# Optimization experiments

Measured on AMD Instinct MI355X. Metric: run time of the kernel, lower is better.

The kernel has to match this reference:

```python
import jax, jax.numpy as jnp
import numpy as np

DECAY = 0.999
EPS = 1e-05
COMMIT = 0.25


def _layer_norm(x, g, b, eps=1e-5):
    mu = x.mean(-1, keepdims=True)
    var = ((x - mu) ** 2).mean(-1, keepdims=True)
    return (x - mu) * jax.lax.rsqrt(var + eps) * g + b


def setup_inputs() -> dict:
    key = jax.random.key(0)
    ks = jax.random.split(key, 8)
    B, T, D, M, H = 8, 4096, 512, 1024, 512
    init_bound = 1.0 / 512
    embedding = jax.random.uniform(ks[0], (M, D), jnp.float32, -init_bound, init_bound)
    return {
        "dense_x": jax.random.normal(ks[1], (B, T, D), jnp.float32),
        "dense_padding_mask": jax.random.randint(ks[2], (B, T), 0, 2).astype(bool),
        "labels": jax.random.randint(ks[3], (B, T), 0, M),
        "embedding": embedding,
        "ema_count": jnp.zeros((M,), jnp.float32),
        "ema_weight": embedding,
        "ln1_g": jnp.ones((D,), jnp.float32),
        "ln1_b": jnp.zeros((D,), jnp.float32),
        "W1": jax.random.normal(ks[4], (D, H), jnp.float32) * (1.0 / np.sqrt(D)),
        "ln2_g": jnp.ones((H,), jnp.float32),
        "ln2_b": jnp.zeros((H,), jnp.float32),
        "W2": jax.random.normal(ks[5], (H, M), jnp.float32) * (1.0 / np.sqrt(H)),
    }


def reference(dense_x, dense_padding_mask, labels, embedding, ema_count, ema_weight,
              ln1_g, ln1_b, W1, ln2_g, ln2_b, W2):
    B, T, D = dense_x.shape
    M = embedding.shape[0]
    N = B * T

    # ---- VQ codebook (EMA) ----
    x_flat = jax.lax.stop_gradient(dense_x).reshape(N, D)
    distances = (jnp.sum(embedding ** 2, axis=1)[None, :]
                 + jnp.sum(x_flat ** 2, axis=1, keepdims=True)
                 - 2.0 * (x_flat @ embedding.T))
    indices = jnp.argmin(distances, axis=-1)  # [N]
    quantized = embedding[indices].reshape(B, T, D)

    # EMA codebook update (training path); encodings.sum(0) and encodings.T @ x
    # expressed as scatter-adds instead of materializing [N, M] one-hot.
    counts = jnp.zeros((M,), dense_x.dtype).at[indices].add(1.0)
    new_count = DECAY * ema_count + (1.0 - DECAY) * counts
    n = jnp.sum(new_count)
    new_count = (new_count + EPS) / (n + M * EPS) * n
    dw = jnp.zeros((M, D), dense_x.dtype).at[indices].add(x_flat)
    new_weight = DECAY * ema_weight + (1.0 - DECAY) * dw
    new_embedding = new_weight / new_count[:, None]

    e_latent_loss = (dense_x - jax.lax.stop_gradient(quantized)) ** 2  # [B,T,D]
    vq_loss = COMMIT * e_latent_loss
    quantized_st = dense_x + jax.lax.stop_gradient(quantized - dense_x)

    avg_probs = counts / N
    perplexity = jnp.exp(-jnp.sum(avg_probs * jnp.log(avg_probs + 1e-10)))

    # ---- decoder: LN -> ReLU -> Linear -> LN -> ReLU -> Linear ----
    h = jax.nn.relu(_layer_norm(dense_x, ln1_g, ln1_b)) @ W1      # [B,T,H]
    logits = jax.nn.relu(_layer_norm(h, ln2_g, ln2_b)) @ W2       # [B,T,M]

    # ---- cross-entropy with ignore_index=-1 (padding) ----
    lab = jnp.where(dense_padding_mask, -1, labels)
    valid = lab >= 0
    safe = jnp.where(valid, lab, 0)
    logp = jax.nn.log_softmax(logits, axis=-1)
    ce = -jnp.take_along_axis(logp, safe[..., None], axis=-1)[..., 0]
    recon_loss = jnp.where(valid, ce, 0.0)

    loss = recon_loss + vq_loss.sum(-1)  # [B,T]
    return quantized_st, loss, perplexity, new_embedding, new_count, new_weight
```

## Files before the change

kernel.cpp:

```cpp
#include <hip/hip_runtime.h>


#define N_TOK 32768

typedef __attribute__((ext_vector_type(8))) short short8;
typedef _Float16 half8 __attribute__((ext_vector_type(8)));
typedef __attribute__((ext_vector_type(4))) float f32x4;

__device__ __forceinline__ f32x4 mfma16(short8 a, short8 b, f32x4 c) {
    return __builtin_amdgcn_mfma_f32_16x16x32_bf16(a, b, c, 0, 0, 0);
}
__device__ __forceinline__ f32x4 mfma16h(half8 a, half8 b, f32x4 c) {
    return __builtin_amdgcn_mfma_f32_16x16x32_f16(a, b, c, 0, 0, 0);
}

__device__ __forceinline__ void gl_lds16(const void* g, void* l) {
    __builtin_amdgcn_global_load_lds(
        (const __attribute__((address_space(1))) void*)g,
        (__attribute__((address_space(3))) void*)l, 16, 0, 0);
}

__device__ __forceinline__ unsigned short f2bf(float x) {
    unsigned u = __float_as_uint(x);
    u += 0x7fffu + ((u >> 16) & 1u);
    return (unsigned short)(u >> 16);
}
__device__ __forceinline__ float bf2f(unsigned short h) {
    return __uint_as_float(((unsigned)h) << 16);
}
__device__ __forceinline__ unsigned short f2h(float x) {
    union { _Float16 h; unsigned short u; } c;
    c.h = (_Float16)x;
    return c.u;
}
__device__ __forceinline__ float h2f(unsigned short u) {
    union { _Float16 h; unsigned short u; } c;
    c.u = u;
    return (float)c.h;
}

__device__ __forceinline__ float waveSum(float v) {
#pragma unroll
    for (int off = 32; off > 0; off >>= 1) v += __shfl_down(v, off, 64);
    return v;
}
__device__ __forceinline__ float xorSum(float v) {
#pragma unroll
    for (int off = 1; off < 64; off <<= 1) v += __shfl_xor(v, off);
    return v;
}

__device__ __forceinline__ void stage_tile128(const unsigned short* __restrict__ src,
                                              int r0, int k0, short* lds,
                                              int w, int lane) {
#pragma unroll
    for (int iss = 0; iss < 2; ++iss) {
        int L = (w << 11) + (iss << 10) + (lane << 4);
        int kb = L >> 11, m = (L >> 4) & 127;
        gl_lds16(src + (((size_t)(r0 + m)) << 9) + k0 + (kb << 3), (char*)lds + L);
    }
}

__global__ __launch_bounds__(256) void prep_x_kernel(
        const float* __restrict__ X, const float* __restrict__ g,
        const float* __restrict__ b, unsigned short* __restrict__ Xf,
        unsigned short* __restrict__ A1) {
    int lane = threadIdx.x & 63;
    int n = (blockIdx.x << 2) + (threadIdx.x >> 6);
    const float* row = X + ((size_t)n << 9);
    float v[8]; float s = 0.f, ss = 0.f;
#pragma unroll
    for (int i = 0; i < 8; ++i) { v[i] = row[lane + (i << 6)]; s += v[i]; ss += v[i] * v[i]; }
    s = xorSum(s); ss = xorSum(ss);
    float mu = s * (1.f / 512.f);
    float rs = rsqrtf(ss * (1.f / 512.f) - mu * mu + 1e-5f);
#pragma unroll
    for (int i = 0; i < 8; ++i) {
        int c = lane + (i << 6);
        size_t o = ((size_t)n << 9) + c;
        float x = v[i];
        Xf[o] = f2h(x);
        float a = fmaxf((x - mu) * rs * g[c] + b[c], 0.f);
        A1[o] = f2bf(a);
    }
}

__global__ __launch_bounds__(256) void prep_h_kernel(
        const unsigned short* __restrict__ Hb, const float* __restrict__ g,
        const float* __restrict__ b, unsigned short* __restrict__ A2) {
    int lane = threadIdx.x & 63;
    int n = (blockIdx.x << 2) + (threadIdx.x >> 6);
    const unsigned short* row = Hb + ((size_t)n << 9);
    float v[8]; float s = 0.f, ss = 0.f;
#pragma unroll
    for (int i = 0; i < 8; ++i) { v[i] = bf2f(row[lane + (i << 6)]); s += v[i]; ss += v[i] * v[i]; }
    s = xorSum(s); ss = xorSum(ss);
    float mu = s * (1.f / 512.f);
    float rs = rsqrtf(ss * (1.f / 512.f) - mu * mu + 1e-5f);
#pragma unroll
    for (int i = 0; i < 8; ++i) {
        int c = lane + (i << 6);
        float a = fmaxf((v[i] - mu) * rs * g[c] + b[c], 0.f);
        A2[((size_t)n << 9) + c] = f2bf(a);
    }
}

__global__ __launch_bounds__(256) void prep_e_kernel(
        const float* __restrict__ E, unsigned short* __restrict__ Ehf,
        unsigned short* __restrict__ Elf, float* __restrict__ e_sq) {
    int lane = threadIdx.x & 63;
    int m = (blockIdx.x << 2) + (threadIdx.x >> 6);
    const float* row = E + ((size_t)m << 9);
    float ss = 0.f;
#pragma unroll
    for (int i = 0; i < 8; ++i) {
        int c = lane + (i << 6);
        float x = row[c];
        ss += x * x;
        float xs = x * 512.f;
        unsigned short h = f2h(xs);
        size_t o = ((size_t)m << 9) + c;
        Ehf[o] = h;
        Elf[o] = f2h(xs - h2f(h));
    }
    ss = xorSum(ss);
    if (lane == 0) e_sq[m] = ss * 512.f;
}

__global__ __launch_bounds__(256) void prep_wt_kernel(
        const float* __restrict__ W, unsigned short* __restrict__ WT, int Nw) {
    __shared__ float t[32][33];
    int n0 = blockIdx.x << 5, k0 = blockIdx.y << 5;
    int tx = threadIdx.x & 31, ty = threadIdx.x >> 5;
#pragma unroll
    for (int l = 0; l < 4; ++l)
        t[ty + (l << 3)][tx] = W[(size_t)(k0 + ty + (l << 3)) * Nw + n0 + tx];
    __syncthreads();
#pragma unroll
    for (int l = 0; l < 4; ++l)
        WT[(((size_t)(n0 + ty + (l << 3))) << 9) + k0 + tx] = f2bf(t[tx][ty + (l << 3)]);
}

__device__ __forceinline__ unsigned long long packDist(float d, int m) {
    unsigned u = __float_as_uint(d);
    u = (u & 0x80000000u) ? ~u : (u | 0x80000000u);
    return ((unsigned long long)u << 32) | (unsigned)m;
}

__global__ __launch_bounds__(256) void dist_mfma_kernel(
        const unsigned short* __restrict__ Xf,
        const unsigned short* __restrict__ Ehf, const unsigned short* __restrict__ Elf,
        const float* __restrict__ e_sq, unsigned long long* __restrict__ minpack) {
    __shared__ __align__(16) short Axs[4096], Bh[4096], Bl[4096];
    int tid = threadIdx.x, lane = tid & 63, w = tid >> 6;
    int quad = lane >> 4, lanelo = lane & 15;
    int wm = w >> 1, wn = w & 1;
    int row0 = blockIdx.x << 7, m0 = blockIdx.y << 7;
    f32x4 acc[4][4];
#pragma unroll
    for (int i = 0; i < 4; ++i)
#pragma unroll
        for (int j = 0; j < 4; ++j) acc[i][j] = 0.f;

    for (int k0 = 0; k0 < 512; k0 += 32) {
        stage_tile128(Xf, row0, k0, Axs, w, lane);
        stage_tile128(Ehf, m0, k0, Bh, w, lane);
        stage_tile128(Elf, m0, k0, Bl, w, lane);
        __syncthreads();
        half8 av[4], bh[4], bl[4];
#pragma unroll
        for (int i = 0; i < 4; ++i) {
            int m = (wm << 6) + (i << 4) + lanelo;
            av[i] = __builtin_bit_cast(half8, *(const short8*)&Axs[(quad << 10) + (m << 3)]);
        }
#pragma unroll
        for (int j = 0; j < 4; ++j) {
            int n = (wn << 6) + (j << 4) + lanelo;
            bh[j] = __builtin_bit_cast(half8, *(const short8*)&Bh[(quad << 10) + (n << 3)]);
            bl[j] = __builtin_bit_cast(half8, *(const short8*)&Bl[(quad << 10) + (n << 3)]);
        }
#pragma unroll
        for (int i = 0; i < 4; ++i)
#pragma unroll
            for (int j = 0; j < 4; ++j) {
                acc[i][j] = mfma16h(av[i], bh[j], acc[i][j]);
                acc[i][j] = mfma16h(av[i], bl[j], acc[i][j]);
            }
        __syncthreads();
    }

    float esq[4];
#pragma unroll
    for (int j = 0; j < 4; ++j) esq[j] = e_sq[m0 + (wn << 6) + (j << 4) + lanelo];
#pragma unroll
    for (int i = 0; i < 4; ++i)
#pragma unroll
        for (int r = 0; r < 4; ++r) {
            unsigned long long best = ~0ULL;
#pragma unroll
            for (int j = 0; j < 4; ++j) {
                int code = m0 + (wn << 6) + (j << 4) + lanelo;
                float d = esq[j] - 2.f * acc[i][j][r];
                unsigned long long p = packDist(d, code);
                if (p < best) best = p;
            }
#pragma unroll
            for (int off = 1; off < 16; off <<= 1) {
                unsigned long long q = __shfl_xor(best, off);
                if (q < best) best = q;
            }
            if (lanelo == 0) {
                int t = row0 + (wm << 6) + (i << 4) + (quad << 2) + r;
                atomicMin(&minpack[t], best);
            }
        }
}

__global__ __launch_bounds__(256) void gather_kernel(
        const float* __restrict__ X, const float* __restrict__ E,
        const unsigned long long* __restrict__ minpack,
        float* __restrict__ out_q, int* __restrict__ icounts,
        float* __restrict__ vqsum) {
    int lane = threadIdx.x & 63;
    int n = (blockIdx.x << 2) + (threadIdx.x >> 6);
    int idx = (int)(minpack[n] & 0xFFFFFFFFULL);
    if (lane == 0) atomicAdd(&icounts[idx], 1);
    const float* xr = X + ((size_t)n << 9);
    const float* er = E + ((size_t)idx << 9);
    float s = 0.f;
#pragma unroll
    for (int i = 0; i < 8; ++i) {
        int c = lane + (i << 6);
        float xv = xr[c], q = er[c];
        out_q[((size_t)n << 9) + c] = q;
        float dlt = xv - q;
        s += dlt * dlt;
    }
    s = waveSum(s);
    if (lane == 0) vqsum[n] = 0.25f * s;
}

__global__ __launch_bounds__(1024) void codebook_kernel(
        const float* __restrict__ ema_count, const int* __restrict__ icounts,
        float* __restrict__ out_perp, float* __restrict__ out_newcount,
        int* __restrict__ offsets) {
    __shared__ int sc[1024];
    __shared__ float red[16];
    int tid = threadIdx.x;
    int lane = tid & 63, wid = tid >> 6;
    int ic = icounts[tid];
    sc[tid] = ic;
    for (int off = 1; off < 1024; off <<= 1) {
        __syncthreads();
        int v = (tid >= off) ? sc[tid - off] : 0;
        __syncthreads();
        sc[tid] += v;
    }
    offsets[tid] = sc[tid] - ic;
    __syncthreads();

    float cnt = (float)ic;
    float raw = 0.999f * ema_count[tid] + 0.001f * cnt;
    float v = waveSum(raw);
    if (lane == 0) red[wid] = v;
    __syncthreads();
    float nsum = 0.f;
#pragma unroll
    for (int i = 0; i < 16; ++i) nsum += red[i];
    __syncthreads();
    float p = cnt * (1.f / 32768.f);
    float e = p * logf(p + 1e-10f);
    e = waveSum(e);
    if (lane == 0) red[wid] = e;
    __syncthreads();
    float ent = 0.f;
#pragma unroll
    for (int i = 0; i < 16; ++i) ent += red[i];
    float nc = (raw + 1e-5f) / (nsum + 1024.f * 1e-5f) * nsum;
    out_newcount[tid] = nc;
    if (tid == 0) out_perp[0] = expf(-ent);
}

__global__ __launch_bounds__(256) void scatter_kernel(
        const unsigned long long* __restrict__ minpack,
        const int* __restrict__ offsets, int* __restrict__ cursor,
        int* __restrict__ bucket) {
    int n = (blockIdx.x << 8) + threadIdx.x;
    int idx = (int)(minpack[n] & 0xFFFFFFFFULL);
    int pos = atomicAdd(&cursor[idx], 1);
    bucket[offsets[idx] + pos] = n;
}

__global__ __launch_bounds__(256) void dw_kernel(
        const float* __restrict__ X, const int* __restrict__ bucket,
        const int* __restrict__ icounts, const int* __restrict__ offsets,
        float* __restrict__ dw) {
    __shared__ float comb[4][512];
    int tid = threadIdx.x, lane = tid & 63, w = tid >> 6;
    int m = blockIdx.x;
    int cnt = icounts[m], base = offsets[m];
    float acc[8] = {};
    for (int i = w; i < cnt; i += 4) {
        int t = bucket[base + i];
        const float* xr = X + ((size_t)t << 9);
#pragma unroll
        for (int j = 0; j < 8; ++j) acc[j] += xr[lane + (j << 6)];
    }
#pragma unroll
    for (int j = 0; j < 8; ++j) comb[w][lane + (j << 6)] = acc[j];
    __syncthreads();
    for (int c = tid; c < 512; c += 256)
        dw[((size_t)m << 9) + c] = comb[0][c] + comb[1][c] + comb[2][c] + comb[3][c];
}

__global__ __launch_bounds__(256) void gemm1_mfma_kernel(
        const unsigned short* __restrict__ A1, const unsigned short* __restrict__ W1T,
        unsigned short* __restrict__ Hb) {
    __shared__ __align__(16) short As[4096], Bs[4096];
    int tid = threadIdx.x, lane = tid & 63, w = tid >> 6;
    int quad = lane >> 4, lanelo = lane & 15;
    int wm = w >> 1, wn = w & 1;
    int row0 = blockIdx.x << 7, n0 = blockIdx.y << 7;
    f32x4 acc[4][4];
#pragma unroll
    for (int i = 0; i < 4; ++i)
#pragma unroll
        for (int j = 0; j < 4; ++j) acc[i][j] = 0.f;

    for (int k0 = 0; k0 < 512; k0 += 32) {
        stage_tile128(A1, row0, k0, As, w, lane);
        stage_tile128(W1T, n0, k0, Bs, w, lane);
        __syncthreads();
        short8 af[4], bf[4];
#pragma unroll
        for (int i = 0; i < 4; ++i) {
            int m = (wm << 6) + (i << 4) + lanelo;
            af[i] = *(const short8*)&As[(quad << 10) + (m << 3)];
        }
#pragma unroll
        for (int j = 0; j < 4; ++j) {
            int n = (wn << 6) + (j << 4) + lanelo;
            bf[j] = *(const short8*)&Bs[(quad << 10) + (n << 3)];
        }
#pragma unroll
        for (int i = 0; i < 4; ++i)
#pragma unroll
            for (int j = 0; j < 4; ++j) acc[i][j] = mfma16(af[i], bf[j], acc[i][j]);
        __syncthreads();
    }
#pragma unroll
    for (int i = 0; i < 4; ++i)
#pragma unroll
        for (int j = 0; j < 4; ++j)
#pragma unroll
            for (int r = 0; r < 4; ++r) {
                int row = row0 + (wm << 6) + (i << 4) + (quad << 2) + r;
                int col = n0 + (wn << 6) + (j << 4) + lanelo;
                Hb[((size_t)row << 9) + col] = f2bf(acc[i][j][r]);
            }
}

__global__ __launch_bounds__(256) void gemm2_chunk_kernel(
        const unsigned short* __restrict__ A2, const unsigned short* __restrict__ W2T,
        const int* __restrict__ mask, const int* __restrict__ labels,
        float* __restrict__ ws_cmax, float* __restrict__ ws_csum,
        float* __restrict__ ws_lab) {
    __shared__ __align__(16) short As[4096], Bs[4096];
    __shared__ float lmax[2][2][64], lsum[2][2][64], llab[128];
    __shared__ int slab[128];
    int tid = threadIdx.x, lane = tid & 63, w = tid >> 6;
    int quad = lane >> 4, lanelo = lane & 15;
    int wm = w >> 1, wn = w & 1;
    int row0 = blockIdx.x << 7, c0 = blockIdx.y << 7;
    if (tid < 128) {
        int mk = mask[row0 + tid];
        slab[tid] = mk ? 0 : labels[row0 + tid];
    }
    f32x4 acc[4][4];
#pragma unroll
    for (int i = 0; i < 4; ++i)
#pragma unroll
        for (int j = 0; j < 4; ++j) acc[i][j] = 0.f;

    for (int k0 = 0; k0 < 512; k0 += 32) {
        stage_tile128(A2, row0, k0, As, w, lane);
        stage_tile128(W2T, c0, k0, Bs, w, lane);
        __syncthreads();
        short8 af[4], bf[4];
#pragma unroll
        for (int i = 0; i < 4; ++i) {
            int m = (wm << 6) + (i << 4) + lanelo;
            af[i] = *(const short8*)&As[(quad << 10) + (m << 3)];
        }
#pragma unroll
        for (int j = 0; j < 4; ++j) {
            int n = (wn << 6) + (j << 4) + lanelo;
            bf[j] = *(const short8*)&Bs[(quad << 10) + (n << 3)];
        }
#pragma unroll
        for (int i = 0; i < 4; ++i)
#pragma unroll
            for (int j = 0; j < 4; ++j) acc[i][j] = mfma16(af[i], bf[j], acc[i][j]);
        __syncthreads();
    }

#pragma unroll
    for (int i = 0; i < 4; ++i)
#pragma unroll
        for (int j = 0; j < 4; ++j)
#pragma unroll
            for (int r = 0; r < 4; ++r) {
                int code = c0 + (wn << 6) + (j << 4) + lanelo;
                int tt = (wm << 6) + (i << 4) + (quad << 2) + r;
                if (code == slab[tt]) llab[tt] = acc[i][j][r];
            }
#pragma unroll
    for (int i = 0; i < 4; ++i)
#pragma unroll
        for (int r = 0; r < 4; ++r) {
            float mx = fmaxf(fmaxf(acc[i][0][r], acc[i][1][r]),
                             fmaxf(acc[i][2][r], acc[i][3][r]));
#pragma unroll
            for (int off = 1; off < 16; off <<= 1) mx = fmaxf(mx, __shfl_xor(mx, off));
            if (lanelo == 0) lmax[wm][wn][(i << 4) + (quad << 2) + r] = mx;
        }
    __syncthreads();
#pragma unroll
    for (int i = 0; i < 4; ++i)
#pragma unroll
        for (int r = 0; r < 4; ++r) {
            int tl = (i << 4) + (quad << 2) + r;
            float cm = fmaxf(lmax[wm][0][tl], lmax[wm][1][tl]);
            float s = expf(acc[i][0][r] - cm) + expf(acc[i][1][r] - cm) +
                      expf(acc[i][2][r] - cm) + expf(acc[i][3][r] - cm);
#pragma unroll
            for (int off = 1; off < 16; off <<= 1) s += __shfl_xor(s, off);
            if (lanelo == 0) lsum[wm][wn][tl] = s;
        }
    __syncthreads();
    if (tid < 128) {
        int wmi = tid >> 6, tl = tid & 63;
        int token = row0 + tid;
        float cm = fmaxf(lmax[wmi][0][tl], lmax[wmi][1][tl]);
        float cs = lsum[wmi][0][tl] + lsum[wmi][1][tl];
        size_t o = ((size_t)blockIdx.y << 15) + token;
        ws_cmax[o] = cm;
        ws_csum[o] = cs;
        if ((slab[tid] >> 7) == (int)blockIdx.y) ws_lab[token] = llab[tid];
    }
}

__global__ __launch_bounds__(256) void ce_combine_kernel(
        const float* __restrict__ ws_cmax, const float* __restrict__ ws_csum,
        const float* __restrict__ ws_lab, const int* __restrict__ mask,
        const float* __restrict__ vqsum, float* __restrict__ loss_out) {
    int n = (blockIdx.x << 8) + threadIdx.x;
    float m[8], s[8];
#pragma unroll
    for (int c = 0; c < 8; ++c) {
        m[c] = ws_cmax[(c << 15) + n];
        s[c] = ws_csum[(c << 15) + n];
    }
    float gm = m[0];
#pragma unroll
    for (int c = 1; c < 8; ++c) gm = fmaxf(gm, m[c]);
    float se = 0.f;
#pragma unroll
    for (int c = 0; c < 8; ++c) se += s[c] * expf(m[c] - gm);
    float ce = -(ws_lab[n] - gm - logf(se));
    loss_out[n] = (mask[n] ? 0.f : ce) + vqsum[n];
}

__global__ __launch_bounds__(256) void newweight_kernel(
        const float* __restrict__ ema_weight, const float* __restrict__ dw,
        const float* __restrict__ newcount, float* __restrict__ out_neww,
        float* __restrict__ out_newemb) {
    int i = (blockIdx.x << 8) + threadIdx.x;
    float nw = 0.999f * ema_weight[i] + 0.001f * dw[i];
    out_neww[i] = nw;
    out_newemb[i] = nw / newcount[i >> 9];
}

extern "C" void kernel_launch(void* const* d_in, const int* in_sizes, int n_in,
                              void* d_out, int out_size, void* d_ws, size_t ws_size,
                              hipStream_t stream) {
    const float* X          = (const float*)d_in[0];
    const int*   mask       = (const int*)d_in[1];
    const int*   labels     = (const int*)d_in[2];
    const float* E          = (const float*)d_in[3];
    const float* ema_count  = (const float*)d_in[4];
    const float* ema_weight = (const float*)d_in[5];
    const float* g1 = (const float*)d_in[6];
    const float* b1 = (const float*)d_in[7];
    const float* W1 = (const float*)d_in[8];
    const float* g2 = (const float*)d_in[9];
    const float* b2 = (const float*)d_in[10];
    const float* W2 = (const float*)d_in[11];

    float* out = (float*)d_out;
    float* out_q        = out;
    float* out_loss     = out + 16777216;
    float* out_perp     = out + 16809984;
    float* out_newemb   = out + 16809985;
    float* out_newcount = out + 17334273;
    float* out_neww     = out + 17335297;

    float* w = (float*)d_ws;
    float* vqsum = w;  w += 32768;
    float* e_sq = w;   w += 1024;
    float* dwbuf = w;  w += 524288;
    unsigned long long* minpack = (unsigned long long*)w; w += 65536;
    float* ws_cmax = w; w += 262144;
    float* ws_csum = w; w += 262144;
    float* ws_lab  = w; w += 32768;
    int* icounts = (int*)w; w += 1024;
    int* cursor  = (int*)w; w += 1024;
    int* offsets = (int*)w; w += 1024;
    int* bucket  = (int*)w; w += 32768;
    unsigned short* Ehf = (unsigned short*)w; w += 262144;
    unsigned short* Elf = (unsigned short*)w; w += 262144;
    unsigned short* W1T = (unsigned short*)w; w += 131072;
    unsigned short* W2T = (unsigned short*)w; w += 262144;
    unsigned short* Xf  = (unsigned short*)w; w += 8388608;
    unsigned short* A1  = (unsigned short*)w; w += 8388608;
    unsigned short* Hb  = (unsigned short*)w; w += 8388608;
    unsigned short* A2  = Xf;

    hipMemsetAsync(icounts, 0, 2048 * sizeof(int), stream);
    hipMemsetAsync(minpack, 0xFF, (size_t)N_TOK * sizeof(unsigned long long), stream);

    prep_e_kernel<<<256, 256, 0, stream>>>(E, Ehf, Elf, e_sq);
    prep_wt_kernel<<<dim3(16, 16), 256, 0, stream>>>(W1, W1T, 512);
    prep_wt_kernel<<<dim3(32, 16), 256, 0, stream>>>(W2, W2T, 1024);
    prep_x_kernel<<<8192, 256, 0, stream>>>(X, g1, b1, Xf, A1);
    dist_mfma_kernel<<<dim3(256, 8), 256, 0, stream>>>(Xf, Ehf, Elf, e_sq, minpack);
    gather_kernel<<<8192, 256, 0, stream>>>(X, E, minpack, out_q, icounts, vqsum);
    codebook_kernel<<<1, 1024, 0, stream>>>(ema_count, icounts, out_perp,
                                            out_newcount, offsets);
    scatter_kernel<<<128, 256, 0, stream>>>(minpack, offsets, cursor, bucket);
    dw_kernel<<<1024, 256, 0, stream>>>(X, bucket, icounts, offsets, dwbuf);
    gemm1_mfma_kernel<<<dim3(256, 4), 256, 0, stream>>>(A1, W1T, Hb);
    prep_h_kernel<<<8192, 256, 0, stream>>>(Hb, g2, b2, A2);
    gemm2_chunk_kernel<<<dim3(256, 8), 256, 0, stream>>>(A2, W2T, mask, labels,
                                                         ws_cmax, ws_csum, ws_lab);
    ce_combine_kernel<<<128, 256, 0, stream>>>(ws_cmax, ws_csum, ws_lab,
                                               mask, vqsum, out_loss);
    newweight_kernel<<<2048, 256, 0, stream>>>(ema_weight, dwbuf, out_newcount,
                                               out_neww, out_newemb);
}
```

Baseline: 491.0 us.

## Load GEMM B operands directly from global and fuse small launches

The dist, gemm1 and gemm2 kernels stop staging the B operand (codebook halves, W1T, W2T) through LDS. Each lane now reads its B fragments straight from global memory with precomputed row offsets, which shrinks LDS use and LDS traffic per iteration. Separately, the two memsets are folded into the prep kernels, the two weight-transpose launches are merged into one, and ce_combine and newweight are merged into a single epilogue kernel to cut launch overhead. The risk is that uncoalesced, L2-dependent global loads of B fragments in the inner loop add latency that is no longer hidden by the LDS staging.

```diff
diff --git a/kernel.cpp b/kernel.cpp
--- a/kernel.cpp
+++ b/kernel.cpp
@@ -64,9 +64,11 @@
 __global__ __launch_bounds__(256) void prep_x_kernel(
         const float* __restrict__ X, const float* __restrict__ g,
         const float* __restrict__ b, unsigned short* __restrict__ Xf,
-        unsigned short* __restrict__ A1) {
-    int lane = threadIdx.x & 63;
-    int n = (blockIdx.x << 2) + (threadIdx.x >> 6);
+        unsigned short* __restrict__ A1, unsigned long long* __restrict__ minpack) {
+    int tid = threadIdx.x;
+    if (tid < 4) minpack[(blockIdx.x << 2) + tid] = ~0ULL;
+    int lane = tid & 63;
+    int n = (blockIdx.x << 2) + (tid >> 6);
     const float* row = X + ((size_t)n << 9);
     float v[8]; float s = 0.f, ss = 0.f;
 #pragma unroll
@@ -107,7 +109,9 @@
 
 __global__ __launch_bounds__(256) void prep_e_kernel(
         const float* __restrict__ E, unsigned short* __restrict__ Ehf,
-        unsigned short* __restrict__ Elf, float* __restrict__ e_sq) {
+        unsigned short* __restrict__ Elf, float* __restrict__ e_sq,
+        int* __restrict__ izero) {
+    if (blockIdx.x < 8) izero[(blockIdx.x << 8) + threadIdx.x] = 0;
     int lane = threadIdx.x & 63;
     int m = (blockIdx.x << 2) + (threadIdx.x >> 6);
     const float* row = E + ((size_t)m << 9);
@@ -128,9 +132,14 @@
 }
 
 __global__ __launch_bounds__(256) void prep_wt_kernel(
-        const float* __restrict__ W, unsigned short* __restrict__ WT, int Nw) {
+        const float* __restrict__ W1, const float* __restrict__ W2,
+        unsigned short* __restrict__ W1T, unsigned short* __restrict__ W2T) {
     __shared__ float t[32][33];
-    int n0 = blockIdx.x << 5, k0 = blockIdx.y << 5;
+    int bx = blockIdx.x;
+    const float* W = (bx < 16) ? W1 : W2;
+    unsigned short* WT = (bx < 16) ? W1T : W2T;
+    int Nw = (bx < 16) ? 512 : 1024;
+    int n0 = ((bx < 16) ? bx : (bx - 16)) << 5, k0 = blockIdx.y << 5;
     int tx = threadIdx.x & 31, ty = threadIdx.x >> 5;
 #pragma unroll
     for (int l = 0; l < 4; ++l)
@@ -151,7 +160,7 @@
         const unsigned short* __restrict__ Xf,
         const unsigned short* __restrict__ Ehf, const unsigned short* __restrict__ Elf,
         const float* __restrict__ e_sq, unsigned long long* __restrict__ minpack) {
-    __shared__ __align__(16) short Axs[4096], Bh[4096], Bl[4096];
+    __shared__ __align__(16) short Axs[4096];
     int tid = threadIdx.x, lane = tid & 63, w = tid >> 6;
     int quad = lane >> 4, lanelo = lane & 15;
     int wm = w >> 1, wn = w & 1;
@@ -162,22 +171,27 @@
 #pragma unroll
         for (int j = 0; j < 4; ++j) acc[i][j] = 0.f;
 
+    size_t boff[4];
+#pragma unroll
+    for (int j = 0; j < 4; ++j) {
+        int code = m0 + (wn << 6) + (j << 4) + lanelo;
+        boff[j] = ((size_t)code << 9) + (quad << 3);
+    }
+
     for (int k0 = 0; k0 < 512; k0 += 32) {
         stage_tile128(Xf, row0, k0, Axs, w, lane);
-        stage_tile128(Ehf, m0, k0, Bh, w, lane);
-        stage_tile128(Elf, m0, k0, Bl, w, lane);
-        __syncthreads();
-        half8 av[4], bh[4], bl[4];
+        half8 bh[4], bl[4];
+#pragma unroll
+        for (int j = 0; j < 4; ++j) {
+            bh[j] = __builtin_bit_cast(half8, *(const short8*)(Ehf + boff[j] + k0));
+            bl[j] = __builtin_bit_cast(half8, *(const short8*)(Elf + boff[j] + k0));
+        }
+        __syncthreads();
+        half8 av[4];
 #pragma unroll
         for (int i = 0; i < 4; ++i) {
             int m = (wm << 6) + (i << 4) + lanelo;
             av[i] = __builtin_bit_cast(half8, *(const short8*)&Axs[(quad << 10) + (m << 3)]);
-        }
-#pragma unroll
-        for (int j = 0; j < 4; ++j) {
-            int n = (wn << 6) + (j << 4) + lanelo;
-            bh[j] = __builtin_bit_cast(half8, *(const short8*)&Bh[(quad << 10) + (n << 3)]);
-            bl[j] = __builtin_bit_cast(half8, *(const short8*)&Bl[(quad << 10) + (n << 3)]);
         }
 #pragma unroll
         for (int i = 0; i < 4; ++i)
@@ -316,7 +330,7 @@
 __global__ __launch_bounds__(256) void gemm1_mfma_kernel(
         const unsigned short* __restrict__ A1, const unsigned short* __restrict__ W1T,
         unsigned short* __restrict__ Hb) {
-    __shared__ __align__(16) short As[4096], Bs[4096];
+    __shared__ __align__(16) short As[4096];
     int tid = threadIdx.x, lane = tid & 63, w = tid >> 6;
     int quad = lane >> 4, lanelo = lane & 15;
     int wm = w >> 1, wn = w & 1;
@@ -327,20 +341,22 @@
 #pragma unroll
         for (int j = 0; j < 4; ++j) acc[i][j] = 0.f;
 
+    size_t boff[4];
+#pragma unroll
+    for (int j = 0; j < 4; ++j)
+        boff[j] = ((size_t)(n0 + (wn << 6) + (j << 4) + lanelo) << 9) + (quad << 3);
+
     for (int k0 = 0; k0 < 512; k0 += 32) {
         stage_tile128(A1, row0, k0, As, w, lane);
-        stage_tile128(W1T, n0, k0, Bs, w, lane);
-        __syncthreads();
-        short8 af[4], bf[4];
+        short8 bf[4];
+#pragma unroll
+        for (int j = 0; j < 4; ++j) bf[j] = *(const short8*)(W1T + boff[j] + k0);
+        __syncthreads();
+        short8 af[4];
 #pragma unroll
         for (int i = 0; i < 4; ++i) {
             int m = (wm << 6) + (i << 4) + lanelo;
             af[i] = *(const short8*)&As[(quad << 10) + (m << 3)];
-        }
-#pragma unroll
-        for (int j = 0; j < 4; ++j) {
-            int n = (wn << 6) + (j << 4) + lanelo;
-            bf[j] = *(const short8*)&Bs[(quad << 10) + (n << 3)];
         }
 #pragma unroll
         for (int i = 0; i < 4; ++i)
@@ -365,7 +381,7 @@
         const int* __restrict__ mask, const int* __restrict__ labels,
         float* __restrict__ ws_cmax, float* __restrict__ ws_csum,
         float* __restrict__ ws_lab) {
-    __shared__ __align__(16) short As[4096], Bs[4096];
+    __shared__ __align__(16) short As[4096];
     __shared__ float lmax[2][2][64], lsum[2][2][64], llab[128];
     __shared__ int slab[128];
     int tid = threadIdx.x, lane = tid & 63, w = tid >> 6;
@@ -382,20 +398,22 @@
 #pragma unroll
         for (int j = 0; j < 4; ++j) acc[i][j] = 0.f;
 
+    size_t boff[4];
+#pragma unroll
+    for (int j = 0; j < 4; ++j)
+        boff[j] = ((size_t)(c0 + (wn << 6) + (j << 4) + lanelo) << 9) + (quad << 3);
+
     for (int k0 = 0; k0 < 512; k0 += 32) {
         stage_tile128(A2, row0, k0, As, w, lane);
-        stage_tile128(W2T, c0, k0, Bs, w, lane);
-        __syncthreads();
-        short8 af[4], bf[4];
+        short8 bf[4];
+#pragma unroll
+        for (int j = 0; j < 4; ++j) bf[j] = *(const short8*)(W2T + boff[j] + k0);
+        __syncthreads();
+        short8 af[4];
 #pragma unroll
         for (int i = 0; i < 4; ++i) {
             int m = (wm << 6) + (i << 4) + lanelo;
             af[i] = *(const short8*)&As[(quad << 10) + (m << 3)];
-        }
-#pragma unroll
-        for (int j = 0; j < 4; ++j) {
-            int n = (wn << 6) + (j << 4) + lanelo;
-            bf[j] = *(const short8*)&Bs[(quad << 10) + (n << 3)];
         }
 #pragma unroll
         for (int i = 0; i < 4; ++i)
@@ -450,35 +468,36 @@
     }
 }
 
-__global__ __launch_bounds__(256) void ce_combine_kernel(
+__global__ __launch_bounds__(256) void epilogue_kernel(
+        const float* __restrict__ ema_weight, const float* __restrict__ dw,
+        const float* __restrict__ newcount, float* __restrict__ out_neww,
+        float* __restrict__ out_newemb,
         const float* __restrict__ ws_cmax, const float* __restrict__ ws_csum,
         const float* __restrict__ ws_lab, const int* __restrict__ mask,
         const float* __restrict__ vqsum, float* __restrict__ loss_out) {
-    int n = (blockIdx.x << 8) + threadIdx.x;
-    float m[8], s[8];
-#pragma unroll
-    for (int c = 0; c < 8; ++c) {
-        m[c] = ws_cmax[(c << 15) + n];
-        s[c] = ws_csum[(c << 15) + n];
-    }
-    float gm = m[0];
-#pragma unroll
-    for (int c = 1; c < 8; ++c) gm = fmaxf(gm, m[c]);
-    float se = 0.f;
-#pragma unroll
-    for (int c = 0; c < 8; ++c) se += s[c] * expf(m[c] - gm);
-    float ce = -(ws_lab[n] - gm - logf(se));
-    loss_out[n] = (mask[n] ? 0.f : ce) + vqsum[n];
-}
-
-__global__ __launch_bounds__(256) void newweight_kernel(
-        const float* __restrict__ ema_weight, const float* __restrict__ dw,
-        const float* __restrict__ newcount, float* __restrict__ out_neww,
-        float* __restrict__ out_newemb) {
-    int i = (blockIdx.x << 8) + threadIdx.x;
-    float nw = 0.999f * ema_weight[i] + 0.001f * dw[i];
-    out_neww[i] = nw;
-    out_newemb[i] = nw / newcount[i >> 9];
+    int bx = blockIdx.x;
+    if (bx < 2048) {
+        int i = (bx << 8) + threadIdx.x;
+        float nw = 0.999f * ema_weight[i] + 0.001f * dw[i];
+        out_neww[i] = nw;
+        out_newemb[i] = nw / newcount[i >> 9];
+    } else {
+        int n = ((bx - 2048) << 8) + threadIdx.x;
+        float m[8], s[8];
+#pragma unroll
+        for (int c = 0; c < 8; ++c) {
+            m[c] = ws_cmax[(c << 15) + n];
+            s[c] = ws_csum[(c << 15) + n];
+        }
+        float gm = m[0];
+#pragma unroll
+        for (int c = 1; c < 8; ++c) gm = fmaxf(gm, m[c]);
+        float se = 0.f;
+#pragma unroll
+        for (int c = 0; c < 8; ++c) se += s[c] * expf(m[c] - gm);
+        float ce = -(ws_lab[n] - gm - logf(se));
+        loss_out[n] = (mask[n] ? 0.f : ce) + vqsum[n];
+    }
 }
 
 extern "C" void kernel_launch(void* const* d_in, const int* in_sizes, int n_in,
@@ -526,13 +545,9 @@
     unsigned short* Hb  = (unsigned short*)w; w += 8388608;
     unsigned short* A2  = Xf;
 
-    hipMemsetAsync(icounts, 0, 2048 * sizeof(int), stream);
-    hipMemsetAsync(minpack, 0xFF, (size_t)N_TOK * sizeof(unsigned long long), stream);
-
-    prep_e_kernel<<<256, 256, 0, stream>>>(E, Ehf, Elf, e_sq);
-    prep_wt_kernel<<<dim3(16, 16), 256, 0, stream>>>(W1, W1T, 512);
-    prep_wt_kernel<<<dim3(32, 16), 256, 0, stream>>>(W2, W2T, 1024);
-    prep_x_kernel<<<8192, 256, 0, stream>>>(X, g1, b1, Xf, A1);
+    prep_e_kernel<<<256, 256, 0, stream>>>(E, Ehf, Elf, e_sq, icounts);
+    prep_wt_kernel<<<dim3(48, 16), 256, 0, stream>>>(W1, W2, W1T, W2T);
+    prep_x_kernel<<<8192, 256, 0, stream>>>(X, g1, b1, Xf, A1, minpack);
     dist_mfma_kernel<<<dim3(256, 8), 256, 0, stream>>>(Xf, Ehf, Elf, e_sq, minpack);
     gather_kernel<<<8192, 256, 0, stream>>>(X, E, minpack, out_q, icounts, vqsum);
     codebook_kernel<<<1, 1024, 0, stream>>>(ema_count, icounts, out_perp,
@@ -543,8 +558,8 @@
     prep_h_kernel<<<8192, 256, 0, stream>>>(Hb, g2, b2, A2);
     gemm2_chunk_kernel<<<dim3(256, 8), 256, 0, stream>>>(A2, W2T, mask, labels,
                                                          ws_cmax, ws_csum, ws_lab);
-    ce_combine_kernel<<<128, 256, 0, stream>>>(ws_cmax, ws_csum, ws_lab,
-                                               mask, vqsum, out_loss);
-    newweight_kernel<<<2048, 256, 0, stream>>>(ema_weight, dwbuf, out_newcount,
-                                               out_neww, out_newemb);
-}
+    epilogue_kernel<<<2176, 256, 0, stream>>>(ema_weight, dwbuf, out_newcount,
+                                              out_neww, out_newemb,
+                                              ws_cmax, ws_csum, ws_lab,
+                                              mask, vqsum, out_loss);
+}
```

After: 560.4 us. 14.1% more time.
